# Optimization experiments

Measured on AMD Instinct MI355X. Metric: run time of the kernel, lower is better.

The kernel has to match this reference:

```python
import jax, jax.numpy as jnp
import numpy as np

N, E, B, D, L, IN, H = 50000, 800000, 64, 64, 4, 7, 4


def _leaky(x, s=0.2):
    return jnp.where(x >= 0, x, s * x)


def _layernorm(x, g, b, eps=1e-5):
    mu = x.mean(-1, keepdims=True)
    v = ((x - mu) ** 2).mean(-1, keepdims=True)
    return (x - mu) * jax.lax.rsqrt(v + eps) * g + b


def _forward(x, edge_index, batch,
             enc_W, enc_b,
             gat_Wl, gat_Wr, gat_att, gat_b,
             ln_g, ln_b, ffn_W1, ffn_b1, ffn_W2, ffn_b2,
             n2g_W1, n2g_b1, n2g_W2, n2g_b2,
             g2n_W1, g2n_b1, g2n_W2, g2n_b2,
             dec_W1, dec_b1, dec_W2, dec_b2):
    n = x.shape[0]
    loops = jnp.arange(n, dtype=edge_index.dtype)
    src = jnp.concatenate([edge_index[0], loops])  # PyG add_self_loops=True
    dst = jnp.concatenate([edge_index[1], loops])

    h = x @ enc_W + enc_b  # encoder [N, D]
    for l in range(L):
        # ---- GATv2Conv(heads=4, concat=False), eval mode (dropout off) ----
        xl = (h @ gat_Wl[l]).reshape(n, H, D)  # source transform (lin_l)
        xr = (h @ gat_Wr[l]).reshape(n, H, D)  # target transform (lin_r)
        s = xl[src] + xr[dst]                              # [Et, H, D]
        e = jnp.sum(_leaky(s) * gat_att[l], axis=-1)       # [Et, H]
        m = jax.ops.segment_max(e, dst, num_segments=n)
        a = jnp.exp(e - m[dst])
        denom = jax.ops.segment_sum(a, dst, num_segments=n)
        a = a / (denom[dst] + 1e-16)                       # segment softmax
        out = jax.ops.segment_sum(a[..., None] * xl[src], dst, num_segments=n)
        out = out.mean(axis=1) + gat_b[l]                  # head average + bias
        # ---- residual + LayerNorm + FFN ----
        h2 = _layernorm(h + out, ln_g[l], ln_b[l])
        h = h2 + (_leaky(h2 @ ffn_W1[l] + ffn_b1[l]) @ ffn_W2[l] + ffn_b2[l])
        # ---- GlobalContextLayer ----
        lat = jax.nn.gelu(h @ n2g_W1[l] + n2g_b1[l]) @ n2g_W2[l] + n2g_b2[l]
        cnt = jax.ops.segment_sum(jnp.ones((n, 1), h.dtype), batch, num_segments=B)
        gmean = jax.ops.segment_sum(lat, batch, num_segments=B) / jnp.maximum(cnt, 1.0)
        gmax = jax.ops.segment_max(lat, batch, num_segments=B)
        gl = jnp.concatenate([gmean, gmax], axis=1)        # [B, 2D]
        ctx = jax.nn.gelu(gl @ g2n_W1[l] + g2n_b1[l]) @ g2n_W2[l] + g2n_b2[l]
        h = h + ctx[batch]
    return jax.nn.gelu(h @ dec_W1 + dec_b1) @ dec_W2 + dec_b2  # [N, 2]


def setup_inputs() -> dict:
    key = jax.random.key(0)
    ks = jax.random.split(key, 16)
    f = lambda i, s: jax.random.normal(ks[i], s, dtype=jnp.float32) * 0.1
    z = lambda s: jnp.zeros(s, jnp.float32)
    return dict(
        x=jax.random.normal(ks[0], (N, IN), dtype=jnp.float32),
        edge_index=jax.random.randint(ks[1], (2, E), 0, N, dtype=jnp.int32),
        batch=jnp.sort(jax.random.randint(ks[2], (N,), 0, B, dtype=jnp.int32)),
        enc_W=f(3, (IN, D)), enc_b=z((D,)),
        gat_Wl=f(4, (L, D, H * D)), gat_Wr=f(5, (L, D, H * D)),
        gat_att=f(6, (L, H, D)), gat_b=z((L, D)),
        ln_g=jnp.ones((L, D), jnp.float32), ln_b=z((L, D)),
        ffn_W1=f(7, (L, D, 2 * D)), ffn_b1=z((L, 2 * D)),
        ffn_W2=f(8, (L, 2 * D, D)), ffn_b2=z((L, D)),
        n2g_W1=f(9, (L, D, D)), n2g_b1=z((L, D)),
        n2g_W2=f(10, (L, D, D)), n2g_b2=z((L, D)),
        g2n_W1=f(11, (L, 2 * D, D)), g2n_b1=z((L, D)),
        g2n_W2=f(12, (L, D, D)), g2n_b2=z((L, D)),
        dec_W1=f(13, (D, D)), dec_b1=z((D,)),
        dec_W2=f(14, (D, 2)), dec_b2=z((2,)),
    )


def reference(x, edge_index, batch, enc_W, enc_b, gat_Wl, gat_Wr, gat_att, gat_b,
              ln_g, ln_b, ffn_W1, ffn_b1, ffn_W2, ffn_b2,
              n2g_W1, n2g_b1, n2g_W2, n2g_b2,
              g2n_W1, g2n_b1, g2n_W2, g2n_b2,
              dec_W1, dec_b1, dec_W2, dec_b2):
    return _forward(x, edge_index, batch, enc_W, enc_b, gat_Wl, gat_Wr, gat_att, gat_b,
                    ln_g, ln_b, ffn_W1, ffn_b1, ffn_W2, ffn_b2,
                    n2g_W1, n2g_b1, n2g_W2, n2g_b2,
                    g2n_W1, g2n_b1, g2n_W2, g2n_b2,
                    dec_W1, dec_b1, dec_W2, dec_b2)
```

## Files before the change

### kernel.cpp

```cpp
#include <hip/hip_runtime.h>
#include <hip/hip_bf16.h>
#include <math.h>

#define NN 50000
#define EE 800000
#define BBATCH 64
#define DDIM 64
#define NLAYER 4
#define NIN 7
#define NHEAD 4

typedef __attribute__((ext_vector_type(8))) short short8v;
typedef __attribute__((ext_vector_type(4))) float f32x4;
typedef __attribute__((ext_vector_type(2))) float v2f;

static __device__ __forceinline__ float wave_sum(float v) {
#pragma unroll
  for (int m = 32; m > 0; m >>= 1) v += __shfl_xor(v, m, 64);
  return v;
}

static __device__ __forceinline__ float gelu_t(float x) {
  float z = 0.7978845608f * (x + 0.044715f * x * x * x);
  float t = 2.f / (1.f + __expf(-2.f * z)) - 1.f;
  return 0.5f * x * (1.f + t);
}

static __device__ __forceinline__ unsigned short f2b(float v) {
  __hip_bfloat16 b = __float2bfloat16(v);
  return *reinterpret_cast<unsigned short*>(&b);
}

static __device__ __forceinline__ unsigned fkey(float x) {
  unsigned u = __builtin_bit_cast(unsigned, x);
  return (u >> 31) ? ~u : (u | 0x80000000u);
}
static __device__ __forceinline__ float fkey_inv(unsigned k) {
  unsigned u = (k & 0x80000000u) ? (k ^ 0x80000000u) : ~k;
  return __builtin_bit_cast(float, u);
}

template <int CTRL>
static __device__ __forceinline__ float dppf(float v) {
  int x = __builtin_amdgcn_mov_dpp(__builtin_bit_cast(int, v), CTRL, 0xF, 0xF, true);
  return __builtin_bit_cast(float, x);
}

static __device__ __forceinline__ v2f up2(unsigned w) {
  v2f r;
  r.x = __builtin_bit_cast(float, w << 16);
  r.y = __builtin_bit_cast(float, w & 0xFFFF0000u);
  return r;
}

static __device__ __forceinline__ short8v pack8(const float* v) {
  short8v r;
#pragma unroll
  for (int j = 0; j < 8; j++) r[j] = (short)f2b(v[j]);
  return r;
}

__global__ void k_init_cnt(int* cnt, int n) {
  int i = blockIdx.x * blockDim.x + threadIdx.x;
  if (i < n) cnt[i] = 1;
}

__global__ void k_count_edges(const int* __restrict__ dst, int e, int* cnt) {
  int i = blockIdx.x * blockDim.x + threadIdx.x;
  if (i < e) atomicAdd(&cnt[dst[i]], 1);
}

__global__ void k_scan_bsum(const int* __restrict__ cnt, int n, int* bsum) {
  __shared__ int red[256];
  int b = blockIdx.x, t = threadIdx.x;
  int s = 0;
  for (int i = b * 1024 + t; i < (b + 1) * 1024; i += 256)
    if (i < n) s += cnt[i];
  red[t] = s;
  __syncthreads();
  for (int o = 128; o > 0; o >>= 1) {
    if (t < o) red[t] += red[t + o];
    __syncthreads();
  }
  if (t == 0) bsum[b] = red[0];
}

__global__ void k_scan_offsets(int* bsum, int nb) {
  if (threadIdx.x == 0 && blockIdx.x == 0) {
    int acc = 0;
    for (int i = 0; i < nb; i++) { int v = bsum[i]; bsum[i] = acc; acc += v; }
  }
}

__global__ void k_scan_final(int* __restrict__ cnt, int n,
                             const int* __restrict__ bsum, int* __restrict__ indptr,
                             int* __restrict__ esrc) {
  __shared__ int lds[256];
  int b = blockIdx.x, t = threadIdx.x;
  int base = b * 1024;
  int v[4];
  int s = 0;
#pragma unroll
  for (int j = 0; j < 4; j++) {
    int i = base + t * 4 + j;
    v[j] = (i < n) ? cnt[i] : 0;
    s += v[j];
  }
  lds[t] = s;
  __syncthreads();
  for (int o = 1; o < 256; o <<= 1) {
    int x = (t >= o) ? lds[t - o] : 0;
    __syncthreads();
    lds[t] += x;
    __syncthreads();
  }
  int run = bsum[b] + lds[t] - s;
#pragma unroll
  for (int j = 0; j < 4; j++) {
    int i = base + t * 4 + j;
    if (i < n) {
      indptr[i] = run;
      esrc[run] = i;
      cnt[i] = run + 1;
    } else if (i == n) {
      indptr[n] = run;
    }
    run += v[j];
  }
}

__global__ void k_csr_fill(const int* __restrict__ src, const int* __restrict__ dst,
                           int e, int* nxt, int* esrc) {
  int i = blockIdx.x * blockDim.x + threadIdx.x;
  if (i < e) {
    int p = atomicAdd(&nxt[dst[i]], 1);
    esrc[p] = src[i];
  }
}

__global__ void k_batch_starts(const int* __restrict__ batch, int n, int nb, int* starts) {
  int i = blockIdx.x * blockDim.x + threadIdx.x;
  if (i >= n) return;
  int b = batch[i];
  if (i == 0) {
    for (int x = 0; x <= b; x++) starts[x] = 0;
  } else {
    int pb = batch[i - 1];
    if (pb != b)
      for (int x = pb + 1; x <= b; x++) starts[x] = i;
  }
  if (i == n - 1) {
    for (int x = b + 1; x <= nb; x++) starts[x] = n;
  }
}

#define SEG_LR (4 * 512 * 64)
#define SEG_F1 (4 * 128 * 64)
#define SEG_F2 (4 * 64 * 128)
#define SEG_N  (4 * 64 * 64)
#define SEG_D  (64 * 64)
#define WPREP_TOTAL (SEG_LR + SEG_F1 + SEG_F2 + 2 * SEG_N + SEG_D)
__global__ void k_wprep_all(const float* __restrict__ Wl, const float* __restrict__ Wr,
                            const float* __restrict__ F1, const float* __restrict__ F2,
                            const float* __restrict__ N1, const float* __restrict__ N2,
                            const float* __restrict__ D1,
                            unsigned short* __restrict__ wLR, unsigned short* __restrict__ wF1,
                            unsigned short* __restrict__ wF2, unsigned short* __restrict__ wN1,
                            unsigned short* __restrict__ wN2, unsigned short* __restrict__ wD1) {
  int idx = blockIdx.x * blockDim.x + threadIdx.x;
  if (idx < SEG_LR) {
    int l = idx / (512 * 64), rem = idx % (512 * 64);
    int c = rem / 64, k = rem % 64;
    float v = (c < 256) ? Wl[(size_t)l * 64 * 256 + k * 256 + c]
                        : Wr[(size_t)l * 64 * 256 + k * 256 + (c - 256)];
    wLR[idx] = f2b(v);
    return;
  }
  idx -= SEG_LR;
  if (idx < SEG_F1) {
    int l = idx / (128 * 64), rem = idx % (128 * 64);
    int c = rem / 64, k = rem % 64;
    wF1[idx] = f2b(F1[(size_t)l * 64 * 128 + k * 128 + c]);
    return;
  }
  idx -= SEG_F1;
  if (idx < SEG_F2) {
    int l = idx / (64 * 128), rem = idx % (64 * 128);
    int c = rem / 128, k = rem % 128;
    wF2[idx] = f2b(F2[(size_t)l * 128 * 64 + k * 64 + c]);
    return;
  }
  idx -= SEG_F2;
  if (idx < SEG_N) {
    int l = idx / (64 * 64), rem = idx % (64 * 64);
    int c = rem / 64, k = rem % 64;
    wN1[idx] = f2b(N1[(size_t)l * 64 * 64 + k * 64 + c]);
    return;
  }
  idx -= SEG_N;
  if (idx < SEG_N) {
    int l = idx / (64 * 64), rem = idx % (64 * 64);
    int c = rem / 64, k = rem % 64;
    wN2[idx] = f2b(N2[(size_t)l * 64 * 64 + k * 64 + c]);
    return;
  }
  idx -= SEG_N;
  if (idx < SEG_D) {
    int c = idx / 64, k = idx % 64;
    wD1[idx] = f2b(D1[k * 64 + c]);
  }
}

__global__ void k_encoder(const float* __restrict__ x, const float* __restrict__ W,
                          const float* __restrict__ bias, float* __restrict__ h, int n) {
  int idx = blockIdx.x * blockDim.x + threadIdx.x;
  if (idx >= n * 64) return;
  int i = idx >> 6, d = idx & 63;
  float acc = bias[d];
#pragma unroll
  for (int k = 0; k < NIN; k++) acc += x[i * NIN + k] * W[k * 64 + d];
  h[idx] = acc;
}

template <bool CTX>
__global__ __launch_bounds__(256) void k_xlr(const float* __restrict__ A,
                                             const float* __restrict__ ctxv,
                                             const int* __restrict__ batch,
                                             const unsigned short* __restrict__ Wt,
                                             unsigned short* __restrict__ Cb, int n) {
  const int lane = threadIdx.x & 63, wave = threadIdx.x >> 6;
  const int row0 = blockIdx.x * 64 + wave * 16;
  const int c0 = blockIdx.y * 64;
  const int karow = (lane >> 4) * 8;
  const int arow0 = row0 + (lane & 15);
  const int arow = arow0 < n ? arow0 : 0;
  const float* ap = A + (size_t)arow * 64;

  float av[16];
  {
    float4 f0 = *(const float4*)(ap + karow);
    float4 f1 = *(const float4*)(ap + karow + 4);
    float4 f2 = *(const float4*)(ap + 32 + karow);
    float4 f3 = *(const float4*)(ap + 32 + karow + 4);
    av[0] = f0.x; av[1] = f0.y; av[2] = f0.z; av[3] = f0.w;
    av[4] = f1.x; av[5] = f1.y; av[6] = f1.z; av[7] = f1.w;
    av[8] = f2.x; av[9] = f2.y; av[10] = f2.z; av[11] = f2.w;
    av[12] = f3.x; av[13] = f3.y; av[14] = f3.z; av[15] = f3.w;
    if (CTX) {
      const float* cp = ctxv + batch[arow] * 64;
      float4 c0v = *(const float4*)(cp + karow);
      float4 c1v = *(const float4*)(cp + karow + 4);
      float4 c2v = *(const float4*)(cp + 32 + karow);
      float4 c3v = *(const float4*)(cp + 32 + karow + 4);
      av[0] += c0v.x; av[1] += c0v.y; av[2] += c0v.z; av[3] += c0v.w;
      av[4] += c1v.x; av[5] += c1v.y; av[6] += c1v.z; av[7] += c1v.w;
      av[8] += c2v.x; av[9] += c2v.y; av[10] += c2v.z; av[11] += c2v.w;
      av[12] += c3v.x; av[13] += c3v.y; av[14] += c3v.z; av[15] += c3v.w;
    }
  }
  short8v a0 = pack8(av), a1 = pack8(av + 8);

#pragma unroll
  for (int cc = 0; cc < 4; cc++) {
    const int c = c0 + cc * 16 + (lane & 15);
    f32x4 t = {0.f, 0.f, 0.f, 0.f};
    t = __builtin_amdgcn_mfma_f32_16x16x32_bf16(a0, *(const short8v*)(Wt + (size_t)c * 64 + karow), t, 0, 0, 0);
    t = __builtin_amdgcn_mfma_f32_16x16x32_bf16(a1, *(const short8v*)(Wt + (size_t)c * 64 + 32 + karow), t, 0, 0, 0);
#pragma unroll
    for (int r = 0; r < 4; r++) {
      const int row = row0 + (lane >> 4) * 4 + r;
      if (row < n) Cb[(size_t)row * 512 + c] = f2b(t[r]);
    }
  }
}

__global__ __launch_bounds__(256) void k_ffn(const unsigned short* __restrict__ A,
                                             const unsigned short* __restrict__ W1t,
                                             const float* __restrict__ b1,
                                             const unsigned short* __restrict__ W2t,
                                             const float* __restrict__ b2,
                                             const float* __restrict__ res,
                                             float* __restrict__ C,
                                             unsigned short* __restrict__ Cb, int n) {
  __shared__ unsigned short tl[4][16 * 136];
  const int lane = threadIdx.x & 63, wave = threadIdx.x >> 6;
  const int row0 = blockIdx.x * 64 + wave * 16;
  const int karow = (lane >> 4) * 8;
  const int arow = row0 + (lane & 15);
  const size_t abase = (size_t)(arow < n ? arow : 0) * 64 + karow;
  short8v a0 = *(const short8v*)(A + abase);
  short8v a1 = *(const short8v*)(A + abase + 32);

#pragma unroll
  for (int cc = 0; cc < 8; cc++) {
    const int c = cc * 16 + (lane & 15);
    f32x4 t = {0.f, 0.f, 0.f, 0.f};
    t = __builtin_amdgcn_mfma_f32_16x16x32_bf16(a0, *(const short8v*)(W1t + (size_t)c * 64 + karow), t, 0, 0, 0);
    t = __builtin_amdgcn_mfma_f32_16x16x32_bf16(a1, *(const short8v*)(W1t + (size_t)c * 64 + 32 + karow), t, 0, 0, 0);
    const float bv = b1[c];
#pragma unroll
    for (int r = 0; r < 4; r++) {
      float v = t[r] + bv;
      v = fmaxf(v, 0.2f * v);
      int rr = (lane >> 4) * 4 + r;
      tl[wave][rr * 136 + c] = f2b(v);
    }
  }
  __syncthreads();

  short8v a2[4];
#pragma unroll
  for (int f = 0; f < 4; f++)
    a2[f] = *(const short8v*)(&tl[wave][(lane & 15) * 136 + f * 32 + karow]);

#pragma unroll
  for (int cc = 0; cc < 4; cc++) {
    const int c = cc * 16 + (lane & 15);
    f32x4 t = {0.f, 0.f, 0.f, 0.f};
#pragma unroll
    for (int f = 0; f < 4; f++)
      t = __builtin_amdgcn_mfma_f32_16x16x32_bf16(a2[f], *(const short8v*)(W2t + (size_t)c * 128 + f * 32 + karow), t, 0, 0, 0);
    const float bv = b2[c];
#pragma unroll
    for (int r = 0; r < 4; r++) {
      const int row = row0 + (lane >> 4) * 4 + r;
      if (row < n) {
        float v = t[r] + bv + res[(size_t)row * 64 + c];
        C[(size_t)row * 64 + c] = v;
        Cb[(size_t)row * 64 + c] = f2b(v);
      }
    }
  }
}

__global__ __launch_bounds__(256) void k_n2g(const unsigned short* __restrict__ A,
                                             const unsigned short* __restrict__ W1t,
                                             const float* __restrict__ b1,
                                             const unsigned short* __restrict__ W2t,
                                             const float* __restrict__ b2,
                                             const int* __restrict__ batch,
                                             float* __restrict__ psum,
                                             unsigned int* __restrict__ pmax, int n) {
  __shared__ unsigned short tl[4][16 * 72];
  __shared__ float s_sum[64];
  __shared__ unsigned s_max[64];
  const int lane = threadIdx.x & 63, wave = threadIdx.x >> 6;
  const int row0b = blockIdx.x * 64;
  const int row0 = row0b + wave * 16;
  const int karow = (lane >> 4) * 8;
  const int arow = row0 + (lane & 15);
  const size_t abase = (size_t)(arow < n ? arow : 0) * 64 + karow;
  if (threadIdx.x < 64) { s_sum[threadIdx.x] = 0.f; s_max[threadIdx.x] = 0u; }
  short8v a0 = *(const short8v*)(A + abase);
  short8v a1 = *(const short8v*)(A + abase + 32);

#pragma unroll
  for (int cc = 0; cc < 4; cc++) {
    const int c = cc * 16 + (lane & 15);
    f32x4 t = {0.f, 0.f, 0.f, 0.f};
    t = __builtin_amdgcn_mfma_f32_16x16x32_bf16(a0, *(const short8v*)(W1t + (size_t)c * 64 + karow), t, 0, 0, 0);
    t = __builtin_amdgcn_mfma_f32_16x16x32_bf16(a1, *(const short8v*)(W1t + (size_t)c * 64 + 32 + karow), t, 0, 0, 0);
    const float bv = b1[c];
#pragma unroll
    for (int r = 0; r < 4; r++) {
      int rr = (lane >> 4) * 4 + r;
      tl[wave][rr * 72 + c] = f2b(gelu_t(t[r] + bv));
    }
  }
  __syncthreads();

  short8v a2[2];
#pragma unroll
  for (int f = 0; f < 2; f++)
    a2[f] = *(const short8v*)(&tl[wave][(lane & 15) * 72 + f * 32 + karow]);

  float pv[4][4];
#pragma unroll
  for (int cc = 0; cc < 4; cc++) {
    const int c = cc * 16 + (lane & 15);
    f32x4 t = {0.f, 0.f, 0.f, 0.f};
    t = __builtin_amdgcn_mfma_f32_16x16x32_bf16(a2[0], *(const short8v*)(W2t + (size_t)c * 64 + karow), t, 0, 0, 0);
    t = __builtin_amdgcn_mfma_f32_16x16x32_bf16(a2[1], *(const short8v*)(W2t + (size_t)c * 64 + 32 + karow), t, 0, 0, 0);
    const float bv = b2[c];
#pragma unroll
    for (int r = 0; r < 4; r++) pv[cc][r] = t[r] + bv;
  }

  const int blo = batch[row0b];
  const int last = row0b + 63 < n ? row0b + 63 : n - 1;
  const int bhi = batch[last];
  if (blo == bhi && row0b + 63 < n) {
#pragma unroll
    for (int cc = 0; cc < 4; cc++) {
      const int c = cc * 16 + (lane & 15);
      float s = pv[cc][0] + pv[cc][1] + pv[cc][2] + pv[cc][3];
      float mx = fmaxf(fmaxf(pv[cc][0], pv[cc][1]), fmaxf(pv[cc][2], pv[cc][3]));
      atomicAdd(&s_sum[c], s);
      atomicMax(&s_max[c], fkey(mx));
    }
    __syncthreads();
    if (threadIdx.x < 64) {
      atomicAdd(&psum[blo * 64 + threadIdx.x], s_sum[threadIdx.x]);
      atomicMax(&pmax[blo * 64 + threadIdx.x], s_max[threadIdx.x]);
    }
  } else {
#pragma unroll
    for (int cc = 0; cc < 4; cc++) {
      const int c = cc * 16 + (lane & 15);
#pragma unroll
      for (int r = 0; r < 4; r++) {
        const int row = row0 + (lane >> 4) * 4 + r;
        if (row < n) {
          const int b = batch[row];
          atomicAdd(&psum[b * 64 + c], pv[cc][r]);
          atomicMax(&pmax[b * 64 + c], fkey(pv[cc][r]));
        }
      }
    }
  }
}

template <bool CTX>
__global__ __launch_bounds__(256) void k_gat(const unsigned short* __restrict__ xlr,
                                             const float* __restrict__ att,
                                             const float* __restrict__ gbias,
                                             const float* __restrict__ lng,
                                             const float* __restrict__ lnb,
                                             const float* __restrict__ h,
                                             const float* __restrict__ ctxv,
                                             const int* __restrict__ batch,
                                             const int* __restrict__ indptr,
                                             const int* __restrict__ esrc,
                                             float* __restrict__ h2,
                                             unsigned short* __restrict__ h2b, int n) {
  const int wave = threadIdx.x >> 6, lane = threadIdx.x & 63;
  const int node = blockIdx.x * 4 + wave;
  if (node >= n) return;
  const int q = lane >> 4, r = lane & 15;
  const int c = r & 3;
  const int doff = (r >> 2) * 64 + c * 16;

  v2f xr2[8], at2[8];
  {
    const uint4* xp = (const uint4*)(xlr + (size_t)node * 512 + 256 + doff);
    uint4 u0 = xp[0], u1 = xp[1];
    unsigned w[8] = {u0.x, u0.y, u0.z, u0.w, u1.x, u1.y, u1.z, u1.w};
#pragma unroll
    for (int j = 0; j < 8; j++) xr2[j] = up2(w[j]);
    const float4* ap = (const float4*)(att + doff);
#pragma unroll
    for (int k = 0; k < 4; k++) {
      float4 a = ap[k];
      at2[2 * k].x = a.x; at2[2 * k].y = a.y;
      at2[2 * k + 1].x = a.z; at2[2 * k + 1].y = a.w;
    }
  }

  v2f acc2[8] = {};
  float den = 0.f;
  const int beg = indptr[node], end = indptr[node + 1];

  int j0 = beg + q;
  int s_cur = esrc[(j0 < end) ? j0 : beg];
  const uint4* xp0 = (const uint4*)(xlr + (size_t)s_cur * 512 + doff);
  uint4 u0 = xp0[0], u1 = xp0[1];
  int jn1 = beg + 4 + q;
  int s_nxt = esrc[(jn1 < end && beg + 4 < end) ? jn1 : beg];

  for (int jb = beg; jb < end; jb += 4) {
    const uint4 cu0 = u0, cu1 = u1;
    const bool cvalid = (jb + q) < end;
    if (jb + 4 < end) {
      const uint4* xpn = (const uint4*)(xlr + (size_t)s_nxt * 512 + doff);
      u0 = xpn[0];
      u1 = xpn[1];
      if (jb + 8 < end) {
        const int jn = jb + 8 + q;
        s_nxt = esrc[(jn < end) ? jn : beg];
      }
    }
    unsigned w[8] = {cu0.x, cu0.y, cu0.z, cu0.w, cu1.x, cu1.y, cu1.z, cu1.w};
    v2f xs2[8];
#pragma unroll
    for (int j = 0; j < 8; j++) xs2[j] = up2(w[j]);
    v2f p2 = {0.f, 0.f};
#pragma unroll
    for (int j = 0; j < 8; j++) {
      v2f t = xs2[j] + xr2[j];
      t = __builtin_elementwise_max(t, t * 0.2f);
      p2 = __builtin_elementwise_fma(t, at2[j], p2);
    }
    float p = p2.x + p2.y;
    p += dppf<0xB1>(p);
    p += dppf<0x4E>(p);
    const float pw = cvalid ? __expf(fminf(p, 60.f)) : 0.f;
    den += pw;
    v2f pwv = {pw, pw};
#pragma unroll
    for (int j = 0; j < 8; j++) acc2[j] = __builtin_elementwise_fma(pwv, xs2[j], acc2[j]);
  }

  float accf[16];
#pragma unroll
  for (int j = 0; j < 8; j++) { accf[2 * j] = acc2[j].x; accf[2 * j + 1] = acc2[j].y; }

  den += __shfl_xor(den, 16, 64);
  den += __shfl_xor(den, 32, 64);
#pragma unroll
  for (int d = 0; d < 16; d++) {
    accf[d] += __shfl_xor(accf[d], 16, 64);
    accf[d] += __shfl_xor(accf[d], 32, 64);
  }

  const float rden = 0.25f / (den + 1e-16f);
  float y[16];
  float s4 = 0.f;
  const float4* hp = (const float4*)(h + (size_t)node * 64 + c * 16);
  const float4* gp = (const float4*)(gbias + c * 16);
  const float4* cp = CTX ? (const float4*)(ctxv + batch[node] * 64 + c * 16) : nullptr;
#pragma unroll
  for (int k = 0; k < 4; k++) {
    float4 hv = hp[k], gv = gp[k];
    if (CTX) {
      float4 cv = cp[k];
      hv.x += cv.x; hv.y += cv.y; hv.z += cv.z; hv.w += cv.w;
    }
    float hf[4] = {hv.x, hv.y, hv.z, hv.w};
    float gf[4] = {gv.x, gv.y, gv.z, gv.w};
#pragma unroll
    for (int d2 = 0; d2 < 4; d2++) {
      int d = 4 * k + d2;
      float v = accf[d] * rden;
      v += dppf<0x124>(v);
      v += dppf<0x128>(v);
      y[d] = hf[d2] + v + gf[d2];
      s4 += y[d];
    }
  }

  const float mu = wave_sum(s4) * (1.f / 1024.f);
  float v4 = 0.f;
  float dv[16];
#pragma unroll
  for (int d = 0; d < 16; d++) {
    dv[d] = y[d] - mu;
    v4 += dv[d] * dv[d];
  }
  const float var = wave_sum(v4) * (1.f / 1024.f);
  const float rstd = rsqrtf(var + 1e-5f);

  if (lane < 4) {
    float4* outp = (float4*)(h2 + (size_t)node * 64 + lane * 16);
    uint2* outb = (uint2*)(h2b + (size_t)node * 64 + lane * 16);
    const float4* lgp = (const float4*)(lng + lane * 16);
    const float4* lbp = (const float4*)(lnb + lane * 16);
#pragma unroll
    for (int k = 0; k < 4; k++) {
      float4 g = lgp[k], b = lbp[k];
      float o0 = dv[4 * k + 0] * rstd * g.x + b.x;
      float o1 = dv[4 * k + 1] * rstd * g.y + b.y;
      float o2 = dv[4 * k + 2] * rstd * g.z + b.z;
      float o3 = dv[4 * k + 3] * rstd * g.w + b.w;
      float4 of; of.x = o0; of.y = o1; of.z = o2; of.w = o3;
      outp[k] = of;
      uint2 pk;
      pk.x = (unsigned int)f2b(o0) | ((unsigned int)f2b(o1) << 16);
      pk.y = (unsigned int)f2b(o2) | ((unsigned int)f2b(o3) << 16);
      outb[k] = pk;
    }
  }
}

__global__ void k_ctx2(const float* __restrict__ psum, const unsigned int* __restrict__ pmax,
                       const int* __restrict__ starts,
                       const float* __restrict__ W1, const float* __restrict__ b1,
                       const float* __restrict__ W2, const float* __restrict__ b2,
                       float* __restrict__ ctx) {
  int b = blockIdx.x;
  int t = threadIdx.x;
  __shared__ float g[128], tt[64];
  int cnt = starts[b + 1] - starts[b];
  if (t < 64) {
    g[t] = psum[b * 64 + t] / fmaxf((float)cnt, 1.0f);
  } else {
    g[t] = fkey_inv(pmax[b * 64 + (t - 64)]);
  }
  __syncthreads();
  if (t < 64) {
    float acc = b1[t];
    for (int k = 0; k < 128; k++) acc += g[k] * W1[k * 64 + t];
    tt[t] = gelu_t(acc);
  }
  __syncthreads();
  if (t < 64) {
    float acc2 = b2[t];
    for (int k = 0; k < 64; k++) acc2 += tt[k] * W2[k * 64 + t];
    ctx[b * 64 + t] = acc2;
  }
}

__global__ __launch_bounds__(256) void k_dec(const float* __restrict__ A,
                                             const float* __restrict__ ctxv,
                                             const int* __restrict__ batch,
                                             const unsigned short* __restrict__ W1t,
                                             const float* __restrict__ b1,
                                             const float* __restrict__ W2,
                                             const float* __restrict__ b2,
                                             float* __restrict__ out, int n) {
  const int lane = threadIdx.x & 63, wave = threadIdx.x >> 6;
  const int row0 = blockIdx.x * 64 + wave * 16;
  const int karow = (lane >> 4) * 8;
  const int arow0 = row0 + (lane & 15);
  const int arow = arow0 < n ? arow0 : 0;
  const float* ap = A + (size_t)arow * 64;
  const float* cp = ctxv + batch[arow] * 64;

  float av[16];
  {
    float4 f0 = *(const float4*)(ap + karow);
    float4 f1 = *(const float4*)(ap + karow + 4);
    float4 f2 = *(const float4*)(ap + 32 + karow);
    float4 f3 = *(const float4*)(ap + 32 + karow + 4);
    float4 c0v = *(const float4*)(cp + karow);
    float4 c1v = *(const float4*)(cp + karow + 4);
    float4 c2v = *(const float4*)(cp + 32 + karow);
    float4 c3v = *(const float4*)(cp + 32 + karow + 4);
    av[0] = f0.x + c0v.x; av[1] = f0.y + c0v.y; av[2] = f0.z + c0v.z; av[3] = f0.w + c0v.w;
    av[4] = f1.x + c1v.x; av[5] = f1.y + c1v.y; av[6] = f1.z + c1v.z; av[7] = f1.w + c1v.w;
    av[8] = f2.x + c2v.x; av[9] = f2.y + c2v.y; av[10] = f2.z + c2v.z; av[11] = f2.w + c2v.w;
    av[12] = f3.x + c3v.x; av[13] = f3.y + c3v.y; av[14] = f3.z + c3v.z; av[15] = f3.w + c3v.w;
  }
  short8v a0 = pack8(av), a1 = pack8(av + 8);

  float o0[4] = {}, o1[4] = {};
#pragma unroll
  for (int cc = 0; cc < 4; cc++) {
    const int cidx = cc * 16 + (lane & 15);
    f32x4 t = {0.f, 0.f, 0.f, 0.f};
    t = __builtin_amdgcn_mfma_f32_16x16x32_bf16(a0, *(const short8v*)(W1t + (size_t)cidx * 64 + karow), t, 0, 0, 0);
    t = __builtin_amdgcn_mfma_f32_16x16x32_bf16(a1, *(const short8v*)(W1t + (size_t)cidx * 64 + 32 + karow), t, 0, 0, 0);
    const float bv = b1[cidx];
    const float w0 = W2[cidx * 2 + 0], w1 = W2[cidx * 2 + 1];
#pragma unroll
    for (int r = 0; r < 4; r++) {
      float v = gelu_t(t[r] + bv);
      o0[r] = fmaf(v, w0, o0[r]);
      o1[r] = fmaf(v, w1, o1[r]);
    }
  }
#pragma unroll
  for (int m = 1; m < 16; m <<= 1) {
#pragma unroll
    for (int r = 0; r < 4; r++) {
      o0[r] += __shfl_xor(o0[r], m, 64);
      o1[r] += __shfl_xor(o1[r], m, 64);
    }
  }
  if ((lane & 15) == 0) {
#pragma unroll
    for (int r = 0; r < 4; r++) {
      const int row = row0 + (lane >> 4) * 4 + r;
      if (row < n) {
        out[2 * row] = o0[r] + b2[0];
        out[2 * row + 1] = o1[r] + b2[1];
      }
    }
  }
}

extern "C" void kernel_launch(void* const* d_in, const int* in_sizes, int n_in,
                              void* d_out, int out_size, void* d_ws, size_t ws_size,
                              hipStream_t stream) {
  const float* x = (const float*)d_in[0];
  const int* ei = (const int*)d_in[1];
  const int* batch = (const int*)d_in[2];
  const float* enc_W = (const float*)d_in[3];
  const float* enc_b = (const float*)d_in[4];
  const float* gat_Wl = (const float*)d_in[5];
  const float* gat_Wr = (const float*)d_in[6];
  const float* gat_att = (const float*)d_in[7];
  const float* gat_b = (const float*)d_in[8];
  const float* ln_g = (const float*)d_in[9];
  const float* ln_b = (const float*)d_in[10];
  const float* ffn_W1 = (const float*)d_in[11];
  const float* ffn_b1 = (const float*)d_in[12];
  const float* ffn_W2 = (const float*)d_in[13];
  const float* ffn_b2 = (const float*)d_in[14];
  const float* n2g_W1 = (const float*)d_in[15];
  const float* n2g_b1 = (const float*)d_in[16];
  const float* n2g_W2 = (const float*)d_in[17];
  const float* n2g_b2 = (const float*)d_in[18];
  const float* g2n_W1 = (const float*)d_in[19];
  const float* g2n_b1 = (const float*)d_in[20];
  const float* g2n_W2 = (const float*)d_in[21];
  const float* g2n_b2 = (const float*)d_in[22];
  const float* dec_W1 = (const float*)d_in[23];
  const float* dec_b1 = (const float*)d_in[24];
  const float* dec_W2 = (const float*)d_in[25];
  const float* dec_b2 = (const float*)d_in[26];

  const int N = NN, E = EE;
  const int* e_src = ei;
  const int* e_dst = ei + E;

  float* h = (float*)d_ws;
  float* h2 = h + (size_t)N * 64;
  float* ctx = h2 + (size_t)N * 64;
  float* psum_all = ctx + BBATCH * 64;
  unsigned int* pmax_all = (unsigned int*)(psum_all + 4 * BBATCH * 64);
  int* cnt = (int*)(pmax_all + 4 * BBATCH * 64);
  int* indptr = cnt + N;
  int* esrc = indptr + N + 1;
  int* bsum = esrc + (E + N);
  int* starts = bsum + 64;
  size_t off = (size_t)(starts + BBATCH + 1) - (size_t)d_ws;
  off = (off + 15) & ~(size_t)15;
  unsigned short* hb = (unsigned short*)((char*)d_ws + off);
  unsigned short* h2b = hb + (size_t)N * 64;
  unsigned short* xlr = h2b + (size_t)N * 64;
  unsigned short* wLR = xlr + (size_t)N * 512;
  unsigned short* wF1 = wLR + SEG_LR;
  unsigned short* wF2 = wF1 + SEG_F1;
  unsigned short* wN1 = wF2 + SEG_F2;
  unsigned short* wN2 = wN1 + SEG_N;
  unsigned short* wD1 = wN2 + SEG_N;

  const int TPB = 256;
  const int NBLK_SCAN = (N + 1 + 1023) / 1024;

  hipLaunchKernelGGL(k_wprep_all, dim3((WPREP_TOTAL + 255) / 256), dim3(256), 0, stream,
                     gat_Wl, gat_Wr, ffn_W1, ffn_W2, n2g_W1, n2g_W2, dec_W1,
                     wLR, wF1, wF2, wN1, wN2, wD1);

  hipLaunchKernelGGL(k_init_cnt, dim3((N + TPB - 1) / TPB), dim3(TPB), 0, stream, cnt, N);
  hipLaunchKernelGGL(k_count_edges, dim3((E + TPB - 1) / TPB), dim3(TPB), 0, stream, e_dst, E, cnt);
  hipLaunchKernelGGL(k_scan_bsum, dim3(NBLK_SCAN), dim3(256), 0, stream, cnt, N, bsum);
  hipLaunchKernelGGL(k_scan_offsets, dim3(1), dim3(64), 0, stream, bsum, NBLK_SCAN);
  hipLaunchKernelGGL(k_scan_final, dim3(NBLK_SCAN), dim3(256), 0, stream, cnt, N, bsum, indptr, esrc);
  hipLaunchKernelGGL(k_csr_fill, dim3((E + TPB - 1) / TPB), dim3(TPB), 0, stream, e_src, e_dst, E, cnt, esrc);
  hipLaunchKernelGGL(k_batch_starts, dim3((N + TPB - 1) / TPB), dim3(TPB), 0, stream, batch, N, BBATCH, starts);

  hipMemsetAsync(psum_all, 0, 4 * BBATCH * 64 * (sizeof(float) + sizeof(unsigned int)), stream);

  hipLaunchKernelGGL(k_encoder, dim3((N * 64 + TPB - 1) / TPB), dim3(TPB), 0, stream,
                     x, enc_W, enc_b, h, N);

  const int GN = (N + 63) / 64;

  for (int l = 0; l < NLAYER; l++) {
    const unsigned short* LRt = wLR + (size_t)l * 512 * 64;
    const unsigned short* F1t = wF1 + (size_t)l * 128 * 64;
    const unsigned short* F2t = wF2 + (size_t)l * 64 * 128;
    const unsigned short* N1t = wN1 + (size_t)l * 64 * 64;
    const unsigned short* N2t = wN2 + (size_t)l * 64 * 64;
    const float* attl = gat_att + (size_t)l * 256;
    const float* gbl = gat_b + (size_t)l * 64;
    const float* lngl = ln_g + (size_t)l * 64;
    const float* lnbl = ln_b + (size_t)l * 64;
    const float* fb1 = ffn_b1 + (size_t)l * 128;
    const float* fb2 = ffn_b2 + (size_t)l * 64;
    const float* nb1 = n2g_b1 + (size_t)l * 64;
    const float* nb2 = n2g_b2 + (size_t)l * 64;
    const float* gW1 = g2n_W1 + (size_t)l * 128 * 64;
    const float* gb1 = g2n_b1 + (size_t)l * 64;
    const float* gW2 = g2n_W2 + (size_t)l * 64 * 64;
    const float* gb2 = g2n_b2 + (size_t)l * 64;
    float* psumL = psum_all + (size_t)l * BBATCH * 64;
    unsigned int* pmaxL = pmax_all + (size_t)l * BBATCH * 64;

    if (l == 0)
      hipLaunchKernelGGL((k_xlr<false>), dim3(GN, 8), dim3(256), 0, stream,
                         h, nullptr, nullptr, LRt, xlr, N);
    else
      hipLaunchKernelGGL((k_xlr<true>), dim3(GN, 8), dim3(256), 0, stream,
                         h, ctx, batch, LRt, xlr, N);
    if (l == 0)
      hipLaunchKernelGGL((k_gat<false>), dim3((N + 3) / 4), dim3(256), 0, stream,
                         xlr, attl, gbl, lngl, lnbl, h, nullptr, nullptr, indptr, esrc, h2, h2b, N);
    else
      hipLaunchKernelGGL((k_gat<true>), dim3((N + 3) / 4), dim3(256), 0, stream,
                         xlr, attl, gbl, lngl, lnbl, h, ctx, batch, indptr, esrc, h2, h2b, N);
    hipLaunchKernelGGL(k_ffn, dim3(GN), dim3(256), 0, stream,
                       h2b, F1t, fb1, F2t, fb2, h2, h, hb, N);
    hipLaunchKernelGGL(k_n2g, dim3(GN), dim3(256), 0, stream,
                       hb, N1t, nb1, N2t, nb2, batch, psumL, pmaxL, N);
    hipLaunchKernelGGL(k_ctx2, dim3(BBATCH), dim3(128), 0, stream,
                       psumL, pmaxL, starts, gW1, gb1, gW2, gb2, ctx);
  }

  hipLaunchKernelGGL(k_dec, dim3(GN), dim3(256), 0, stream,
                     h, ctx, batch, wD1, dec_b1, dec_W2, dec_b2, (float*)d_out, N);
}
```

Baseline: 879.0 us.

## Make GAT kernel grid-stride persistent and drop packed v2f math

```diff
diff --git a/kernel.cpp b/kernel.cpp
--- a/kernel.cpp
+++ b/kernel.cpp
@@ -12,7 +12,6 @@
 
 typedef __attribute__((ext_vector_type(8))) short short8v;
 typedef __attribute__((ext_vector_type(4))) float f32x4;
-typedef __attribute__((ext_vector_type(2))) float v2f;
 
 static __device__ __forceinline__ float wave_sum(float v) {
 #pragma unroll
@@ -46,11 +45,13 @@
   return __builtin_bit_cast(float, x);
 }
 
-static __device__ __forceinline__ v2f up2(unsigned w) {
-  v2f r;
-  r.x = __builtin_bit_cast(float, w << 16);
-  r.y = __builtin_bit_cast(float, w & 0xFFFF0000u);
-  return r;
+static __device__ __forceinline__ void unpack8(uint4 u, float* xs) {
+  unsigned int w[4] = {u.x, u.y, u.z, u.w};
+#pragma unroll
+  for (int k = 0; k < 4; k++) {
+    xs[2 * k]     = __builtin_bit_cast(float, w[k] << 16);
+    xs[2 * k + 1] = __builtin_bit_cast(float, w[k] & 0xFFFF0000u);
+  }
 }
 
 static __device__ __forceinline__ short8v pack8(const float* v) {
@@ -420,6 +421,7 @@
   }
 }
 
+#define GAT_BLOCKS 2048
 template <bool CTX>
 __global__ __launch_bounds__(256) void k_gat(const unsigned short* __restrict__ xlr,
                                              const float* __restrict__ att,
@@ -434,139 +436,137 @@
                                              float* __restrict__ h2,
                                              unsigned short* __restrict__ h2b, int n) {
   const int wave = threadIdx.x >> 6, lane = threadIdx.x & 63;
-  const int node = blockIdx.x * 4 + wave;
-  if (node >= n) return;
   const int q = lane >> 4, r = lane & 15;
   const int c = r & 3;
   const int doff = (r >> 2) * 64 + c * 16;
 
-  v2f xr2[8], at2[8];
+  float att_d[16];
   {
-    const uint4* xp = (const uint4*)(xlr + (size_t)node * 512 + 256 + doff);
-    uint4 u0 = xp[0], u1 = xp[1];
-    unsigned w[8] = {u0.x, u0.y, u0.z, u0.w, u1.x, u1.y, u1.z, u1.w};
-#pragma unroll
-    for (int j = 0; j < 8; j++) xr2[j] = up2(w[j]);
     const float4* ap = (const float4*)(att + doff);
 #pragma unroll
     for (int k = 0; k < 4; k++) {
       float4 a = ap[k];
-      at2[2 * k].x = a.x; at2[2 * k].y = a.y;
-      at2[2 * k + 1].x = a.z; at2[2 * k + 1].y = a.w;
-    }
-  }
-
-  v2f acc2[8] = {};
-  float den = 0.f;
-  const int beg = indptr[node], end = indptr[node + 1];
-
-  int j0 = beg + q;
-  int s_cur = esrc[(j0 < end) ? j0 : beg];
-  const uint4* xp0 = (const uint4*)(xlr + (size_t)s_cur * 512 + doff);
-  uint4 u0 = xp0[0], u1 = xp0[1];
-  int jn1 = beg + 4 + q;
-  int s_nxt = esrc[(jn1 < end && beg + 4 < end) ? jn1 : beg];
-
-  for (int jb = beg; jb < end; jb += 4) {
-    const uint4 cu0 = u0, cu1 = u1;
-    const bool cvalid = (jb + q) < end;
-    if (jb + 4 < end) {
-      const uint4* xpn = (const uint4*)(xlr + (size_t)s_nxt * 512 + doff);
-      u0 = xpn[0];
-      u1 = xpn[1];
-      if (jb + 8 < end) {
-        const int jn = jb + 8 + q;
-        s_nxt = esrc[(jn < end) ? jn : beg];
+      att_d[4 * k] = a.x; att_d[4 * k + 1] = a.y;
+      att_d[4 * k + 2] = a.z; att_d[4 * k + 3] = a.w;
+    }
+  }
+
+  for (int node = blockIdx.x * 4 + wave; node < n; node += GAT_BLOCKS * 4) {
+    float xr_d[16];
+    {
+      const uint4* xp = (const uint4*)(xlr + (size_t)node * 512 + 256 + doff);
+      uint4 u0 = xp[0], u1 = xp[1];
+      unpack8(u0, xr_d);
+      unpack8(u1, xr_d + 8);
+    }
+
+    float acc[16] = {};
+    float den = 0.f;
+    const int beg = indptr[node], end = indptr[node + 1];
+
+    int j0 = beg + q;
+    int s_cur = esrc[(j0 < end) ? j0 : beg];
+    const uint4* xp0 = (const uint4*)(xlr + (size_t)s_cur * 512 + doff);
+    uint4 u0 = xp0[0], u1 = xp0[1];
+    int jn1 = beg + 4 + q;
+    int s_nxt = esrc[(jn1 < end && beg + 4 < end) ? jn1 : beg];
+
+    for (int jb = beg; jb < end; jb += 4) {
+      const uint4 cu0 = u0, cu1 = u1;
+      const bool cvalid = (jb + q) < end;
+      if (jb + 4 < end) {
+        const uint4* xpn = (const uint4*)(xlr + (size_t)s_nxt * 512 + doff);
+        u0 = xpn[0];
+        u1 = xpn[1];
+        if (jb + 8 < end) {
+          const int jn = jb + 8 + q;
+          s_nxt = esrc[(jn < end) ? jn : beg];
+        }
       }
-    }
-    unsigned w[8] = {cu0.x, cu0.y, cu0.z, cu0.w, cu1.x, cu1.y, cu1.z, cu1.w};
-    v2f xs2[8];
-#pragma unroll
-    for (int j = 0; j < 8; j++) xs2[j] = up2(w[j]);
-    v2f p2 = {0.f, 0.f};
-#pragma unroll
-    for (int j = 0; j < 8; j++) {
-      v2f t = xs2[j] + xr2[j];
-      t = __builtin_elementwise_max(t, t * 0.2f);
-      p2 = __builtin_elementwise_fma(t, at2[j], p2);
-    }
-    float p = p2.x + p2.y;
-    p += dppf<0xB1>(p);
-    p += dppf<0x4E>(p);
-    const float pw = cvalid ? __expf(fminf(p, 60.f)) : 0.f;
-    den += pw;
-    v2f pwv = {pw, pw};
-#pragma unroll
-    for (int j = 0; j < 8; j++) acc2[j] = __builtin_elementwise_fma(pwv, xs2[j], acc2[j]);
-  }
-
-  float accf[16];
-#pragma unroll
-  for (int j = 0; j < 8; j++) { accf[2 * j] = acc2[j].x; accf[2 * j + 1] = acc2[j].y; }
-
-  den += __shfl_xor(den, 16, 64);
-  den += __shfl_xor(den, 32, 64);
-#pragma unroll
-  for (int d = 0; d < 16; d++) {
-    accf[d] += __shfl_xor(accf[d], 16, 64);
-    accf[d] += __shfl_xor(accf[d], 32, 64);
-  }
-
-  const float rden = 0.25f / (den + 1e-16f);
-  float y[16];
-  float s4 = 0.f;
-  const float4* hp = (const float4*)(h + (size_t)node * 64 + c * 16);
-  const float4* gp = (const float4*)(gbias + c * 16);
-  const float4* cp = CTX ? (const float4*)(ctxv + batch[node] * 64 + c * 16) : nullptr;
-#pragma unroll
-  for (int k = 0; k < 4; k++) {
-    float4 hv = hp[k], gv = gp[k];
-    if (CTX) {
-      float4 cv = cp[k];
-      hv.x += cv.x; hv.y += cv.y; hv.z += cv.z; hv.w += cv.w;
-    }
-    float hf[4] = {hv.x, hv.y, hv.z, hv.w};
-    float gf[4] = {gv.x, gv.y, gv.z, gv.w};
-#pragma unroll
-    for (int d2 = 0; d2 < 4; d2++) {
-      int d = 4 * k + d2;
-      float v = accf[d] * rden;
-      v += dppf<0x124>(v);
-      v += dppf<0x128>(v);
-      y[d] = hf[d2] + v + gf[d2];
-      s4 += y[d];
-    }
-  }
-
-  const float mu = wave_sum(s4) * (1.f / 1024.f);
-  float v4 = 0.f;
-  float dv[16];
-#pragma unroll
-  for (int d = 0; d < 16; d++) {
-    dv[d] = y[d] - mu;
-    v4 += dv[d] * dv[d];
-  }
-  const float var = wave_sum(v4) * (1.f / 1024.f);
-  const float rstd = rsqrtf(var + 1e-5f);
-
-  if (lane < 4) {
-    float4* outp = (float4*)(h2 + (size_t)node * 64 + lane * 16);
-    uint2* outb = (uint2*)(h2b + (size_t)node * 64 + lane * 16);
-    const float4* lgp = (const float4*)(lng + lane * 16);
-    const float4* lbp = (const float4*)(lnb + lane * 16);
+      float xs[16];
+      unpack8(cu0, xs);
+      unpack8(cu1, xs + 8);
+      float p0 = 0.f, p1 = 0.f, p2 = 0.f, p3 = 0.f;
+#pragma unroll
+      for (int k = 0; k < 4; k++) {
+        float t0 = xs[4 * k + 0] + xr_d[4 * k + 0]; t0 = fmaxf(t0, 0.2f * t0); p0 = fmaf(t0, att_d[4 * k + 0], p0);
+        float t1 = xs[4 * k + 1] + xr_d[4 * k + 1]; t1 = fmaxf(t1, 0.2f * t1); p1 = fmaf(t1, att_d[4 * k + 1], p1);
+        float t2 = xs[4 * k + 2] + xr_d[4 * k + 2]; t2 = fmaxf(t2, 0.2f * t2); p2 = fmaf(t2, att_d[4 * k + 2], p2);
+        float t3 = xs[4 * k + 3] + xr_d[4 * k + 3]; t3 = fmaxf(t3, 0.2f * t3); p3 = fmaf(t3, att_d[4 * k + 3], p3);
+      }
+      float p = (p0 + p1) + (p2 + p3);
+      p += dppf<0xB1>(p);
+      p += dppf<0x4E>(p);
+      const float pw = cvalid ? __expf(fminf(p, 60.f)) : 0.f;
+      den += pw;
+#pragma unroll
+      for (int d = 0; d < 16; d++) acc[d] = fmaf(pw, xs[d], acc[d]);
+    }
+
+    den += __shfl_xor(den, 16, 64);
+    den += __shfl_xor(den, 32, 64);
+#pragma unroll
+    for (int d = 0; d < 16; d++) {
+      acc[d] += __shfl_xor(acc[d], 16, 64);
+      acc[d] += __shfl_xor(acc[d], 32, 64);
+    }
+
+    const float rden = 0.25f / (den + 1e-16f);
+    float y[16];
+    float s4 = 0.f;
+    const float4* hp = (const float4*)(h + (size_t)node * 64 + c * 16);
+    const float4* gp = (const float4*)(gbias + c * 16);
+    const float4* cp = CTX ? (const float4*)(ctxv + batch[node] * 64 + c * 16) : nullptr;
 #pragma unroll
     for (int k = 0; k < 4; k++) {
-      float4 g = lgp[k], b = lbp[k];
-      float o0 = dv[4 * k + 0] * rstd * g.x + b.x;
-      float o1 = dv[4 * k + 1] * rstd * g.y + b.y;
-      float o2 = dv[4 * k + 2] * rstd * g.z + b.z;
-      float o3 = dv[4 * k + 3] * rstd * g.w + b.w;
-      float4 of; of.x = o0; of.y = o1; of.z = o2; of.w = o3;
-      outp[k] = of;
-      uint2 pk;
-      pk.x = (unsigned int)f2b(o0) | ((unsigned int)f2b(o1) << 16);
-      pk.y = (unsigned int)f2b(o2) | ((unsigned int)f2b(o3) << 16);
-      outb[k] = pk;
+      float4 hv = hp[k], gv = gp[k];
+      if (CTX) {
+        float4 cv = cp[k];
+        hv.x += cv.x; hv.y += cv.y; hv.z += cv.z; hv.w += cv.w;
+      }
+      float hf[4] = {hv.x, hv.y, hv.z, hv.w};
+      float gf[4] = {gv.x, gv.y, gv.z, gv.w};
+#pragma unroll
+      for (int d2 = 0; d2 < 4; d2++) {
+        int d = 4 * k + d2;
+        float v = acc[d] * rden;
+        v += dppf<0x124>(v);
+        v += dppf<0x128>(v);
+        y[d] = hf[d2] + v + gf[d2];
+        s4 += y[d];
+      }
+    }
+
+    const float mu = wave_sum(s4) * (1.f / 1024.f);
+    float v4 = 0.f;
+    float dv[16];
+#pragma unroll
+    for (int d = 0; d < 16; d++) {
+      dv[d] = y[d] - mu;
+      v4 += dv[d] * dv[d];
+    }
+    const float var = wave_sum(v4) * (1.f / 1024.f);
+    const float rstd = rsqrtf(var + 1e-5f);
+
+    if (lane < 4) {
+      float4* outp = (float4*)(h2 + (size_t)node * 64 + lane * 16);
+      uint2* outb = (uint2*)(h2b + (size_t)node * 64 + lane * 16);
+      const float4* lgp = (const float4*)(lng + lane * 16);
+      const float4* lbp = (const float4*)(lnb + lane * 16);
+#pragma unroll
+      for (int k = 0; k < 4; k++) {
+        float4 g = lgp[k], b = lbp[k];
+        float o0 = dv[4 * k + 0] * rstd * g.x + b.x;
+        float o1 = dv[4 * k + 1] * rstd * g.y + b.y;
+        float o2 = dv[4 * k + 2] * rstd * g.z + b.z;
+        float o3 = dv[4 * k + 3] * rstd * g.w + b.w;
+        float4 of; of.x = o0; of.y = o1; of.z = o2; of.w = o3;
+        outp[k] = of;
+        uint2 pk;
+        pk.x = (unsigned int)f2b(o0) | ((unsigned int)f2b(o1) << 16);
+        pk.y = (unsigned int)f2b(o2) | ((unsigned int)f2b(o3) << 16);
+        outb[k] = pk;
+      }
     }
   }
 }
@@ -775,10 +775,10 @@
       hipLaunchKernelGGL((k_xlr<true>), dim3(GN, 8), dim3(256), 0, stream,
                          h, ctx, batch, LRt, xlr, N);
     if (l == 0)
-      hipLaunchKernelGGL((k_gat<false>), dim3((N + 3) / 4), dim3(256), 0, stream,
+      hipLaunchKernelGGL((k_gat<false>), dim3(GAT_BLOCKS), dim3(256), 0, stream,
                          xlr, attl, gbl, lngl, lnbl, h, nullptr, nullptr, indptr, esrc, h2, h2b, N);
     else
-      hipLaunchKernelGGL((k_gat<true>), dim3((N + 3) / 4), dim3(256), 0, stream,
+      hipLaunchKernelGGL((k_gat<true>), dim3(GAT_BLOCKS), dim3(256), 0, stream,
                          xlr, attl, gbl, lngl, lnbl, h, ctx, batch, indptr, esrc, h2, h2b, N);
     hipLaunchKernelGGL(k_ffn, dim3(GN), dim3(256), 0, stream,
                        h2b, F1t, fb1, F2t, fb2, h2, h, hb, N);
```

New measurement: 879.7 us. Within noise of the previous version (+0.1%).
